# Kernel tuning notes

Measured on AMD Instinct MI355X. Metric: run time of the kernel, lower is better.

Reference implementation:

```python
import jax, jax.numpy as jnp
import numpy as np

N_USERS = 20000
N_ITEMS = 20000
H0, H1, H2 = 256, 512, 256  # hidden = [256, 512, 256]
B = 4096
LN_EPS = 1e-5


def _ln(x, g, b):
    m = jnp.mean(x, axis=-1, keepdims=True)
    v = jnp.mean(jnp.square(x - m), axis=-1, keepdims=True)
    return (x - m) * jax.lax.rsqrt(v + LN_EPS) * g + b


def setup_inputs() -> dict:
    key = jax.random.key(0)
    ks = jax.random.split(key, 12)
    s = 0.02
    inp = {
        "user_idx": jax.random.randint(ks[0], (B,), 0, N_USERS),
        "item_idx": jax.random.randint(ks[1], (B,), 0, N_ITEMS),
        # (n_users+1, n_items+1) binary interaction matrix, stored as bool
        "interactions": jax.random.bernoulli(ks[2], 0.05, (N_USERS + 1, N_ITEMS + 1)),
        # proj_u / proj_i (bias=False), torch Linear layout (out, in)
        "Wu": jax.random.normal(ks[3], (H0, N_ITEMS), jnp.float32) * s,
        "Wi": jax.random.normal(ks[4], (H0, N_USERS), jnp.float32) * s,
        # rep_u: Linear(H0,H1)+LN+ReLU, Linear(H1,H2)+LN+ReLU (dropout=eval identity)
        "W1": jax.random.normal(ks[5], (H1, H0), jnp.float32) * s,
        "b1": jnp.zeros((H1,), jnp.float32),
        "g1": jnp.ones((H1,), jnp.float32),
        "be1": jnp.zeros((H1,), jnp.float32),
        "W2": jax.random.normal(ks[6], (H2, H1), jnp.float32) * s,
        "b2": jnp.zeros((H2,), jnp.float32),
        "g2": jnp.ones((H2,), jnp.float32),
        "be2": jnp.zeros((H2,), jnp.float32),
        # logit layer
        "Wl": jax.random.normal(ks[7], (1, H2), jnp.float32) * s,
        "bl": jnp.zeros((1,), jnp.float32),
    }
    return inp


def reference(user_idx, item_idx, interactions, Wu, Wi, W1, b1, g1, be1,
              W2, b2, g2, be2, Wl, bl):
    b_arange = jnp.arange(user_idx.shape[0])

    # --- user history embedding: gather row, zero target item, project, MLP ---
    u_slice = interactions[user_idx, :-1].astype(jnp.float32)      # (B, n_items)
    u_slice = u_slice.at[b_arange, item_idx].set(0.0)
    u = u_slice @ Wu.T                                             # (B, H0)
    u = jax.nn.relu(_ln(u @ W1.T + b1, g1, be1))                   # (B, H1)
    user_rep = jax.nn.relu(_ln(u @ W2.T + b2, g2, be2))            # (B, H2)

    # --- item history embedding: gather column, zero target user, project ---
    i_slice = interactions.T[item_idx][:, :-1].astype(jnp.float32)  # (B, n_users)
    i_slice = i_slice.at[b_arange, user_idx].set(0.0)
    item_rep = i_slice @ Wi.T                                      # (B, H0); rep_i is an empty Sequential in source

    pred_vector = user_rep * item_rep                              # (B, H2) == (B, H0)
    logit = (pred_vector @ Wl.T + bl).squeeze(-1)                  # (B,)
    return logit
```

## Files before the change

### kernel.cpp

```cpp
#include <hip/hip_runtime.h>

#define N_USERS 20000
#define N_ITEMS 20000
#define NI1     20001
#define HB      4096
#define H0      256
#define H1      512
#define H2      256
#define PKW     632
#define PKB     (PKW*4)
#define NWF     12501251
#define PADN    20224

typedef unsigned short u16;
typedef unsigned char  u8;
typedef unsigned int   u32;
typedef unsigned long long u64;

typedef __attribute__((ext_vector_type(8))) __bf16 bf16x8;
typedef __attribute__((ext_vector_type(4))) float  f32x4;

__device__ __forceinline__ u16 f2bf(float f) {
  u32 u = __float_as_uint(f);
  u32 r = (u + 0x7FFFu + ((u >> 16) & 1u)) >> 16;
  return (u16)r;
}

__device__ __forceinline__ void gload16(const u16* gp, u16* lp) {
  __builtin_amdgcn_global_load_lds(
      (const __attribute__((address_space(1))) u32*)gp,
      (__attribute__((address_space(3))) u32*)lp, 16, 0, 0);
}

__global__ __launch_bounds__(256) void k_detect(const u8* __restrict__ inter,
                                                int* __restrict__ flag) {
  __shared__ u32 cnt[4];
  if (threadIdx.x < 4) cnt[threadIdx.x] = 0;
  __syncthreads();
  u32 loc0 = 0, loc1 = 0, loc2 = 0, loc3 = 0;
  for (int i = threadIdx.x; i < 16384; i += 256) {
    u32 w = ((const u32*)inter)[i];
    loc0 += (w & 0x000000FFu) ? 1u : 0u;
    loc1 += (w & 0x0000FF00u) ? 1u : 0u;
    loc2 += (w & 0x00FF0000u) ? 1u : 0u;
    loc3 += (w & 0xFF000000u) ? 1u : 0u;
  }
  atomicAdd(&cnt[0], loc0); atomicAdd(&cnt[1], loc1);
  atomicAdd(&cnt[2], loc2); atomicAdd(&cnt[3], loc3);
  __syncthreads();
  if (threadIdx.x == 0) {
    int lay;
    if (cnt[1] != 0)      lay = 0;
    else if (cnt[0] != 0) lay = 1;
    else                  lay = 2;
    *flag = lay;
  }
}

__global__ __launch_bounds__(256) void k_packF(const u8* __restrict__ inter,
                                               u32* __restrict__ pkF,
                                               const int* __restrict__ flag) {
  int lay = *flag;
  __shared__ u32 nibs[4][8][64];
  const size_t TE = (size_t)NI1 * NI1;
  const int NG = (int)((TE + 8191) / 8192);
  int wave = threadIdx.x >> 6, lane = threadIdx.x & 63;
  const u32* base32 = (const u32*)inter;
  for (int g = blockIdx.x; g < NG; g += gridDim.x) {
    size_t E0 = (size_t)g * 8192 + (size_t)wave * 2048;
    bool full = ((size_t)(g + 1) * 8192) <= TE;
    if (lay != 0) {
      if (full) {
        #pragma unroll
        for (int t = 0; t < 8; ++t) {
          size_t e = E0 + (size_t)t * 256 + lane * 4;
          uint4 v = *(const uint4*)(base32 + e);
          nibs[wave][t][lane] = (v.x ? 1u : 0u) | (v.y ? 2u : 0u) |
                                (v.z ? 4u : 0u) | (v.w ? 8u : 0u);
        }
      } else {
        #pragma unroll
        for (int t = 0; t < 8; ++t) {
          size_t e = E0 + (size_t)t * 256 + lane * 4;
          u32 n = 0;
          #pragma unroll
          for (int c = 0; c < 4; ++c)
            if (e + c < TE && base32[e + c]) n |= 1u << c;
          nibs[wave][t][lane] = n;
        }
      }
    } else {
      #pragma unroll
      for (int t = 0; t < 8; ++t) {
        size_t e = E0 + (size_t)t * 256 + lane * 4;
        u32 n = 0;
        #pragma unroll
        for (int c = 0; c < 4; ++c)
          if (e + c < TE && inter[e + c]) n |= 1u << c;
        nibs[wave][t][lane] = n;
      }
    }
    __syncthreads();
    {
      int t = lane >> 3, j = lane & 7;
      u32 wrd = 0;
      #pragma unroll
      for (int k = 0; k < 8; ++k) wrd |= nibs[wave][t][8 * j + k] << (4 * k);
      size_t wg = (size_t)g * 256 + wave * 64 + lane;
      if (wg < NWF) pkF[wg] = wrd;
    }
    __syncthreads();
  }
}

__global__ __launch_bounds__(256) void k_realign(const u32* __restrict__ pkF,
                                                 u32* __restrict__ pk) {
  int r = blockIdx.x;
  int base = 625 * r + (r >> 5);
  int s = r & 31;
  for (int w = threadIdx.x; w < PKW; w += 256) {
    u32 val = 0;
    if (w < 625) {
      u32 lo = pkF[base + w];
      u32 hi = pkF[base + w + 1];
      val = s ? ((lo >> s) | (hi << (32 - s))) : lo;
    }
    pk[(size_t)r * PKW + w] = val;
  }
}

#define HDSTEP(J, M)                                      \
  _Pragma("unroll")                                       \
  for (int k = 0; k < 32; ++k) if (!(k & J)) {            \
    u32 tt = (a[k] ^ (a[k | J] >> J)) & M;                \
    a[k] ^= tt; a[k | J] ^= tt << J;                      \
  }

__global__ __launch_bounds__(256) void k_bitT(const u32* __restrict__ pk,
                                              u32* __restrict__ pkT) {
  __shared__ u32 buf[512 * 17];
  int t = threadIdx.x;
  int vt = blockIdx.x % 40, wt = blockIdx.x / 40;
  int v0 = vt * 16, wc0 = wt * 16;
  int lw = t & 15, lr = t >> 4;
  for (int ch = 0; ch < 32; ++ch) {
    int rloc = ch * 16 + lr;
    int R = v0 * 32 + rloc;
    int W = wc0 + lw;
    u32 val = 0;
    if (R < N_USERS && W < PKW) val = pk[(size_t)R * PKW + W];
    buf[rloc * 17 + lw] = val;
  }
  __syncthreads();
  u32 a[32];
  #pragma unroll
  for (int j = 0; j < 32; ++j) a[j] = buf[(lr * 32 + j) * 17 + lw];
  HDSTEP(16, 0x0000FFFFu)
  HDSTEP(8,  0x00FF00FFu)
  HDSTEP(4,  0x0F0F0F0Fu)
  HDSTEP(2,  0x33333333u)
  HDSTEP(1,  0x55555555u)
  __syncthreads();
  #pragma unroll
  for (int i = 0; i < 32; ++i) buf[(i * 16 + lw) * 17 + lr] = __brev(a[31 - i]);
  __syncthreads();
  for (int ch = 0; ch < 32; ++ch) {
    int rloc = ch * 16 + lr;
    int C = wc0 * 32 + rloc;
    int V = v0 + lw;
    if (C < N_ITEMS && V < PKW)
      pkT[(size_t)C * PKW + V] = buf[((rloc & 31) * 16 + (rloc >> 5)) * 17 + lw];
  }
}

__global__ __launch_bounds__(256) void k_convert2p(const float* __restrict__ Wu,
                                                   const float* __restrict__ Wi,
                                                   u16* __restrict__ Wub,
                                                   u16* __restrict__ Wib) {
  int r = blockIdx.x;
  const float* src = (r < 256) ? Wu : Wi;
  u16* dst = (r < 256) ? Wub : Wib;
  int rr = r & 255;
  src += (size_t)rr * N_ITEMS;
  dst += (size_t)rr * PADN;
  for (int k8 = threadIdx.x * 8; k8 < PADN; k8 += 256 * 8) {
    u64 p = 0;
    if (k8 < N_ITEMS) {
      float4 v0 = *(const float4*)(src + k8);
      float4 v1 = *(const float4*)(src + k8 + 4);
      p = (u64)f2bf(v0.x) | ((u64)f2bf(v0.y) << 16) |
          ((u64)f2bf(v0.z) << 32) | ((u64)f2bf(v0.w) << 48);
      u64 q = (u64)f2bf(v1.x) | ((u64)f2bf(v1.y) << 16) |
              ((u64)f2bf(v1.z) << 32) | ((u64)f2bf(v1.w) << 48);
      ((u64*)(dst + k8))[0] = p;
      ((u64*)(dst + k8))[1] = q;
    } else {
      ((u64*)(dst + k8))[0] = 0;
      ((u64*)(dst + k8))[1] = 0;
    }
  }
}

__global__ __launch_bounds__(256) void k_transpose2(const float* __restrict__ W1,
                                                    float* __restrict__ W1T,
                                                    const float* __restrict__ W2,
                                                    float* __restrict__ W2T) {
  __shared__ float tile[32][33];
  int bid = blockIdx.x;
  const float* in; float* out; int R, C, b;
  if (bid < 128) { in = W1; out = W1T; R = H1; C = H0; b = bid; }
  else           { in = W2; out = W2T; R = H2; C = H1; b = bid - 128; }
  int nbx = C >> 5;
  int bx = b % nbx, by = b / nbx;
  int c0 = bx * 32, r0 = by * 32;
  int lx = threadIdx.x & 31, ly = threadIdx.x >> 5;
  #pragma unroll
  for (int j = 0; j < 4; ++j)
    tile[ly + 8*j][lx] = in[(size_t)(r0 + ly + 8*j) * C + c0 + lx];
  __syncthreads();
  #pragma unroll
  for (int j = 0; j < 4; ++j)
    out[(size_t)(c0 + ly + 8*j) * R + r0 + lx] = tile[lx][ly + 8*j];
}

__global__ __launch_bounds__(1024) void k_sort(const int* __restrict__ item_idx,
                                               int* __restrict__ perm) {
  __shared__ u32 cnt[N_ITEMS];
  __shared__ u32 tsum[1024];
  int t = threadIdx.x;
  for (int i = t; i < N_ITEMS; i += 1024) cnt[i] = 0;
  __syncthreads();
  for (int b = t; b < HB; b += 1024) atomicAdd(&cnt[item_idx[b]], 1u);
  __syncthreads();
  u32 s = 0;
  int base = t * 20;
  for (int j = 0; j < 20; ++j) { int i = base + j; if (i < N_ITEMS) s += cnt[i]; }
  tsum[t] = s;
  __syncthreads();
  for (int off = 1; off < 1024; off <<= 1) {
    u32 v = (t >= off) ? tsum[t - off] : 0u;
    __syncthreads();
    tsum[t] += v;
    __syncthreads();
  }
  u32 run = tsum[t] - s;
  for (int j = 0; j < 20; ++j) {
    int i = base + j;
    if (i < N_ITEMS) { u32 c = cnt[i]; cnt[i] = run; run += c; }
  }
  __syncthreads();
  for (int b = t; b < HB; b += 1024) {
    int v = item_idx[b];
    u32 pos = atomicAdd(&cnt[v], 1u);
    perm[pos] = b;
  }
}

__global__ __launch_bounds__(256, 4) void k_gemm(
    const u32* __restrict__ pk, const u32* __restrict__ pkT,
    const int* __restrict__ user_idx, const int* __restrict__ item_idx,
    const int* __restrict__ perm,
    const u16* __restrict__ Wub, const u16* __restrict__ Wib,
    float* __restrict__ u0, float* __restrict__ u0b,
    float* __restrict__ ir, float* __restrict__ irb) {
  __shared__ __attribute__((aligned(16))) u16 Bls[2][32 * 256];
  __shared__ __attribute__((aligned(16))) uint2 lut8[16];
  __shared__ u32 pbase[128];
  __shared__ int prow[128];

  int bid = blockIdx.x;
  int kh = bid >> 9;
  int mode_item = (bid >> 8) & 1;
  int lid = bid & 255;
  int M0 = (lid >> 3) * 128;
  int N0 = (lid & 7) * 32;
  int tid = threadIdx.x;
  const u16* Wb = mode_item ? Wib : Wub;
  const u8* Pk = (const u8*)(mode_item ? pkT : pk);
  float* Cout = mode_item ? (kh ? irb : ir) : (kh ? u0b : u0);

  if (tid < 16) {
    u32 v = tid;
    lut8[tid].x = ((v & 1u) ? 0x3F80u : 0u) | ((v & 2u) ? 0x3F800000u : 0u);
    lut8[tid].y = ((v & 4u) ? 0x3F80u : 0u) | ((v & 8u) ? 0x3F800000u : 0u);
  }
  if (tid < 128) {
    int s = M0 + tid;
    if (mode_item) { int p = perm[s]; prow[tid] = p; pbase[tid] = (u32)item_idx[p] * PKB; }
    else           { prow[tid] = s;   pbase[tid] = (u32)user_idx[s] * PKB; }
  }
  __syncthreads();

  f32x4 acc[2][2];
  #pragma unroll
  for (int a = 0; a < 2; ++a)
    #pragma unroll
    for (int b = 0; b < 2; ++b)
      #pragma unroll
      for (int j = 0; j < 4; ++j) acc[a][b][j] = 0.f;

  int lane = tid & 63, wave = tid >> 6;
  int WM = wave * 32;
  int lrow = lane & 15;
  int lk8 = lane >> 4;
  int sh = lk8 * 8;

  u32 pb0 = pbase[WM + lrow];
  u32 pb1 = pbase[WM + 16 + lrow];

  const u16* gsrc[4];
  int ldso[4];
  #pragma unroll
  for (int i = 0; i < 4; ++i) {
    int id = tid + 256 * i;
    int n = id >> 5, c8 = id & 31;
    gsrc[i] = Wb + (size_t)(N0 + n) * PADN + (c8 ^ (n & 7)) * 8;
    ldso[i] = (wave * 64 + 256 * i) * 8;
  }

  int k0_beg = kh ? 10240 : 0;
  int k0_end = kh ? 20224 : 10240;

  #pragma unroll
  for (int i = 0; i < 4; ++i) gload16(gsrc[i] + k0_beg, &Bls[0][ldso[i]]);
  int bc0 = k0_beg >> 3;
  uint4 ca0l = *(const uint4*)(Pk + pb0 + bc0);
  uint4 ca0h = *(const uint4*)(Pk + pb0 + bc0 + 16);
  uint4 ca1l = *(const uint4*)(Pk + pb1 + bc0);
  uint4 ca1h = *(const uint4*)(Pk + pb1 + bc0 + 16);
  __syncthreads();

  int cur = 0;
  for (int k0 = k0_beg; k0 < k0_end; k0 += 256) {
    int k1 = k0 + 256;
    bool more = k1 < k0_end;
    uint4 na0l, na0h, na1l, na1h;
    if (more) {
      #pragma unroll
      for (int i = 0; i < 4; ++i) gload16(gsrc[i] + k1, &Bls[cur ^ 1][ldso[i]]);
      int nbc = k1 >> 3;
      na0l = *(const uint4*)(Pk + pb0 + nbc);
      na0h = *(const uint4*)(Pk + pb0 + nbc + 16);
      na1l = *(const uint4*)(Pk + pb1 + nbc);
      na1h = *(const uint4*)(Pk + pb1 + nbc + 16);
    }
    u32 qw0[8] = {ca0l.x, ca0l.y, ca0l.z, ca0l.w, ca0h.x, ca0h.y, ca0h.z, ca0h.w};
    u32 qw1[8] = {ca1l.x, ca1l.y, ca1l.z, ca1l.w, ca1h.x, ca1h.y, ca1h.z, ca1h.w};
    #pragma unroll
    for (int kki = 0; kki < 8; ++kki) {
      u32 b0 = (qw0[kki] >> sh) & 0xFFu;
      u32 b1 = (qw1[kki] >> sh) & 0xFFu;
      union { u32 w[4]; bf16x8 v; } a0, a1;
      uint2 l0 = lut8[b0 & 15u], h0 = lut8[b0 >> 4];
      uint2 l1 = lut8[b1 & 15u], h1 = lut8[b1 >> 4];
      a0.w[0] = l0.x; a0.w[1] = l0.y; a0.w[2] = h0.x; a0.w[3] = h0.y;
      a1.w[0] = l1.x; a1.w[1] = l1.y; a1.w[2] = h1.x; a1.w[3] = h1.y;
      bf16x8 bfr[2];
      #pragma unroll
      for (int fn = 0; fn < 2; ++fn) {
        int n = fn * 16 + lrow;
        bfr[fn] = *(const bf16x8*)&Bls[cur][n * 256 + ((kki * 32 + sh) ^ ((n & 7) << 3))];
      }
      acc[0][0] = __builtin_amdgcn_mfma_f32_16x16x32_bf16(a0.v, bfr[0], acc[0][0], 0, 0, 0);
      acc[0][1] = __builtin_amdgcn_mfma_f32_16x16x32_bf16(a0.v, bfr[1], acc[0][1], 0, 0, 0);
      acc[1][0] = __builtin_amdgcn_mfma_f32_16x16x32_bf16(a1.v, bfr[0], acc[1][0], 0, 0, 0);
      acc[1][1] = __builtin_amdgcn_mfma_f32_16x16x32_bf16(a1.v, bfr[1], acc[1][1], 0, 0, 0);
    }
    if (more) { ca0l = na0l; ca0h = na0h; ca1l = na1l; ca1h = na1h; }
    __syncthreads();
    cur ^= 1;
  }

  int crow0 = (lane >> 4) * 4;
  int ccol = lane & 15;
  #pragma unroll
  for (int fm = 0; fm < 2; ++fm)
    #pragma unroll
    for (int fn = 0; fn < 2; ++fn) {
      f32x4 v = acc[fm][fn];
      int col = N0 + fn * 16 + ccol;
      #pragma unroll
      for (int j = 0; j < 4; ++j) {
        int rl = WM + fm * 16 + crow0 + j;
        Cout[(size_t)prow[rl] * H0 + col] = v[j];
      }
    }
}

__global__ __launch_bounds__(256) void k_mlp(
    const u32* __restrict__ pk,
    const int* __restrict__ user_idx, const int* __restrict__ item_idx,
    const float* __restrict__ Wu, const float* __restrict__ Wi,
    const float* __restrict__ u0, const float* __restrict__ u0b,
    const float* __restrict__ ir, const float* __restrict__ irb,
    const float* __restrict__ W1T, const float* __restrict__ b1,
    const float* __restrict__ g1, const float* __restrict__ be1,
    const float* __restrict__ W2T, const float* __restrict__ b2,
    const float* __restrict__ g2, const float* __restrict__ be2,
    const float* __restrict__ Wl, const float* __restrict__ bl,
    float* __restrict__ out) {
  __shared__ __attribute__((aligned(16))) float xl[16][H0];
  __shared__ __attribute__((aligned(16))) float h1l[16][H1];
  __shared__ int flagL[16], uL[16], iL[16];

  int tid = threadIdx.x, lane = tid & 63, wave = tid >> 6;
  int b0 = blockIdx.x * 16;

  if (tid < 16) {
    int b = b0 + tid;
    int uu = user_idx[b], ii = item_idx[b];
    uL[tid] = uu; iL[tid] = ii;
    u8 byte = ((const u8*)pk)[(size_t)uu * PKB + (ii >> 3)];
    flagL[tid] = (byte >> (ii & 7)) & 1;
  }
  __syncthreads();

  for (int idx = tid; idx < 16 * H0; idx += 256) {
    int rr = idx >> 8, h = idx & 255;
    size_t o = (size_t)(b0 + rr) * H0 + h;
    float x = u0[o] + u0b[o];
    if (flagL[rr]) x -= Wu[(size_t)h * N_ITEMS + iL[rr]];
    xl[rr][h] = x;
  }
  __syncthreads();

  float a0[16], a1[16];
  #pragma unroll
  for (int rr = 0; rr < 16; ++rr) { a0[rr] = 0.f; a1[rr] = 0.f; }
  for (int k4 = 0; k4 < H0 / 4; ++k4) {
    int k = k4 * 4;
    float w0a = W1T[(size_t)(k+0)*H1 + tid], w0b = W1T[(size_t)(k+0)*H1 + tid + 256];
    float w1a = W1T[(size_t)(k+1)*H1 + tid], w1b = W1T[(size_t)(k+1)*H1 + tid + 256];
    float w2a = W1T[(size_t)(k+2)*H1 + tid], w2b = W1T[(size_t)(k+2)*H1 + tid + 256];
    float w3a = W1T[(size_t)(k+3)*H1 + tid], w3b = W1T[(size_t)(k+3)*H1 + tid + 256];
    #pragma unroll
    for (int rr = 0; rr < 16; ++rr) {
      float4 x = *(const float4*)&xl[rr][k];
      a0[rr] += x.x * w0a + x.y * w1a + x.z * w2a + x.w * w3a;
      a1[rr] += x.x * w0b + x.y * w1b + x.z * w2b + x.w * w3b;
    }
  }
  #pragma unroll
  for (int rr = 0; rr < 16; ++rr) {
    h1l[rr][tid]       = a0[rr] + b1[tid];
    h1l[rr][tid + 256] = a1[rr] + b1[tid + 256];
  }
  __syncthreads();

  for (int rr = wave; rr < 16; rr += 4) {
    float s = 0.f;
    #pragma unroll
    for (int j = 0; j < 8; ++j) s += h1l[rr][lane + 64 * j];
    #pragma unroll
    for (int off = 32; off; off >>= 1) s += __shfl_xor(s, off);
    float m = s * (1.f / H1);
    float v = 0.f;
    #pragma unroll
    for (int j = 0; j < 8; ++j) { float d = h1l[rr][lane + 64*j] - m; v += d * d; }
    #pragma unroll
    for (int off = 32; off; off >>= 1) v += __shfl_xor(v, off);
    float inv = rsqrtf(v * (1.f / H1) + 1e-5f);
    #pragma unroll
    for (int j = 0; j < 8; ++j) {
      int o = lane + 64 * j;
      float y = (h1l[rr][o] - m) * inv * g1[o] + be1[o];
      h1l[rr][o] = fmaxf(y, 0.f);
    }
  }
  __syncthreads();

  float a2[16];
  #pragma unroll
  for (int rr = 0; rr < 16; ++rr) a2[rr] = 0.f;
  for (int k4 = 0; k4 < H1 / 4; ++k4) {
    int k = k4 * 4;
    float w0 = W2T[(size_t)(k+0)*H2 + tid];
    float w1 = W2T[(size_t)(k+1)*H2 + tid];
    float w2 = W2T[(size_t)(k+2)*H2 + tid];
    float w3 = W2T[(size_t)(k+3)*H2 + tid];
    #pragma unroll
    for (int rr = 0; rr < 16; ++rr) {
      float4 x = *(const float4*)&h1l[rr][k];
      a2[rr] += x.x * w0 + x.y * w1 + x.z * w2 + x.w * w3;
    }
  }
  __syncthreads();
  #pragma unroll
  for (int rr = 0; rr < 16; ++rr) xl[rr][tid] = a2[rr] + b2[tid];
  __syncthreads();

  for (int rr = wave; rr < 16; rr += 4) {
    float s = 0.f;
    #pragma unroll
    for (int j = 0; j < 4; ++j) s += xl[rr][lane + 64 * j];
    #pragma unroll
    for (int off = 32; off; off >>= 1) s += __shfl_xor(s, off);
    float m = s * (1.f / H2);
    float v = 0.f;
    #pragma unroll
    for (int j = 0; j < 4; ++j) { float d = xl[rr][lane + 64*j] - m; v += d * d; }
    #pragma unroll
    for (int off = 32; off; off >>= 1) v += __shfl_xor(v, off);
    float inv = rsqrtf(v * (1.f / H2) + 1e-5f);
    #pragma unroll
    for (int j = 0; j < 4; ++j) {
      int o = lane + 64 * j;
      float y = (xl[rr][o] - m) * inv * g2[o] + be2[o];
      xl[rr][o] = fmaxf(y, 0.f);
    }
  }
  __syncthreads();

  for (int rr = wave; rr < 16; rr += 4) {
    int b = b0 + rr;
    int flg = flagL[rr], uu = uL[rr];
    float s = 0.f;
    #pragma unroll
    for (int j = 0; j < 4; ++j) {
      int h = lane + 64 * j;
      size_t o = (size_t)b * H0 + h;
      float irv = ir[o] + irb[o];
      if (flg) irv -= Wi[(size_t)h * N_USERS + uu];
      s += xl[rr][h] * irv * Wl[h];
    }
    #pragma unroll
    for (int off = 32; off; off >>= 1) s += __shfl_xor(s, off);
    if (lane == 0) out[b] = s + bl[0];
  }
}

extern "C" void kernel_launch(void* const* d_in, const int* in_sizes, int n_in,
                              void* d_out, int out_size, void* d_ws, size_t ws_size,
                              hipStream_t stream) {
  const int*   user_idx = (const int*)d_in[0];
  const int*   item_idx = (const int*)d_in[1];
  const u8*    inter    = (const u8*)d_in[2];
  const float* Wu  = (const float*)d_in[3];
  const float* Wi  = (const float*)d_in[4];
  const float* W1  = (const float*)d_in[5];
  const float* b1  = (const float*)d_in[6];
  const float* g1  = (const float*)d_in[7];
  const float* be1 = (const float*)d_in[8];
  const float* W2  = (const float*)d_in[9];
  const float* b2  = (const float*)d_in[10];
  const float* g2  = (const float*)d_in[11];
  const float* be2 = (const float*)d_in[12];
  const float* Wl  = (const float*)d_in[13];
  const float* bl  = (const float*)d_in[14];
  float* out = (float*)d_out;

  char* ws = (char*)d_ws;
  size_t off = 0;
  auto alloc = [&](size_t bytes) {
    size_t o = off;
    off = (off + bytes + 255) & ~(size_t)255;
    return o;
  };
  int*   flag = (int*)  (ws + alloc(4));
  u32*   pkF  = (u32*)  (ws + alloc((size_t)(NWF + 64) * 4));
  u32*   pk   = (u32*)  (ws + alloc((size_t)N_USERS * PKB));
  u32*   pkT  = (u32*)  (ws + alloc((size_t)N_ITEMS * PKB));
  u16*   Wub  = (u16*)  (ws + alloc((size_t)H0 * PADN * 2));
  u16*   Wib  = (u16*)  (ws + alloc((size_t)H0 * PADN * 2));
  float* W1T  = (float*)(ws + alloc((size_t)H0 * H1 * 4));
  float* W2T  = (float*)(ws + alloc((size_t)H1 * H2 * 4));
  float* u0   = (float*)(ws + alloc((size_t)HB * H0 * 4));
  float* u0b  = (float*)(ws + alloc((size_t)HB * H0 * 4));
  float* ir   = (float*)(ws + alloc((size_t)HB * H0 * 4));
  float* irb  = (float*)(ws + alloc((size_t)HB * H0 * 4));
  int*   perm = (int*)  (ws + alloc((size_t)HB * 4));

  k_detect<<<1, 256, 0, stream>>>(inter, flag);
  k_packF<<<3072, 256, 0, stream>>>(inter, pkF, flag);
  k_realign<<<N_USERS, 256, 0, stream>>>(pkF, pk);
  k_bitT<<<1600, 256, 0, stream>>>(pk, pkT);
  k_convert2p<<<512, 256, 0, stream>>>(Wu, Wi, Wub, Wib);
  k_transpose2<<<256, 256, 0, stream>>>(W1, W1T, W2, W2T);
  k_sort<<<1, 1024, 0, stream>>>(item_idx, perm);
  k_gemm<<<1024, 256, 0, stream>>>(pk, pkT, user_idx, item_idx, perm, Wub, Wib,
                                   u0, u0b, ir, irb);
  k_mlp<<<256, 256, 0, stream>>>(pk, user_idx, item_idx, Wu, Wi, u0, u0b, ir, irb,
                                 W1T, b1, g1, be1, W2T, b2, g2, be2, Wl, bl, out);
}
```

Baseline: 630.0 us.

## Split GEMM K dimension four ways with smaller tiles and nontemporal pack loads

The bit-packed GEMM now splits the K reduction into four partitions instead of two and launches 2048 blocks. The per-iteration K step drops from 256 to 128, which halves LDS use and lets the occupancy hint rise from 4 to 6 blocks per CU. The MLP kernel sums four partial outputs instead of two, and the pack kernel reads the large bool matrix with nontemporal loads to avoid cache pollution. In exchange there is more partial-sum traffic and more loop iterations with more barriers per unit of work.

```diff
diff --git a/kernel.cpp b/kernel.cpp
--- a/kernel.cpp
+++ b/kernel.cpp
@@ -19,6 +19,7 @@
 
 typedef __attribute__((ext_vector_type(8))) __bf16 bf16x8;
 typedef __attribute__((ext_vector_type(4))) float  f32x4;
+typedef __attribute__((ext_vector_type(4))) u32    u32x4;
 
 __device__ __forceinline__ u16 f2bf(float f) {
   u32 u = __float_as_uint(f);
@@ -74,7 +75,7 @@
         #pragma unroll
         for (int t = 0; t < 8; ++t) {
           size_t e = E0 + (size_t)t * 256 + lane * 4;
-          uint4 v = *(const uint4*)(base32 + e);
+          u32x4 v = __builtin_nontemporal_load((const u32x4*)(base32 + e));
           nibs[wave][t][lane] = (v.x ? 1u : 0u) | (v.y ? 2u : 0u) |
                                 (v.z ? 4u : 0u) | (v.w ? 8u : 0u);
         }
@@ -184,12 +185,11 @@
   src += (size_t)rr * N_ITEMS;
   dst += (size_t)rr * PADN;
   for (int k8 = threadIdx.x * 8; k8 < PADN; k8 += 256 * 8) {
-    u64 p = 0;
     if (k8 < N_ITEMS) {
       float4 v0 = *(const float4*)(src + k8);
       float4 v1 = *(const float4*)(src + k8 + 4);
-      p = (u64)f2bf(v0.x) | ((u64)f2bf(v0.y) << 16) |
-          ((u64)f2bf(v0.z) << 32) | ((u64)f2bf(v0.w) << 48);
+      u64 p = (u64)f2bf(v0.x) | ((u64)f2bf(v0.y) << 16) |
+              ((u64)f2bf(v0.z) << 32) | ((u64)f2bf(v0.w) << 48);
       u64 q = (u64)f2bf(v1.x) | ((u64)f2bf(v1.y) << 16) |
               ((u64)f2bf(v1.z) << 32) | ((u64)f2bf(v1.w) << 48);
       ((u64*)(dst + k8))[0] = p;
@@ -256,14 +256,16 @@
   }
 }
 
-__global__ __launch_bounds__(256, 4) void k_gemm(
+__global__ __launch_bounds__(256, 6) void k_gemm(
     const u32* __restrict__ pk, const u32* __restrict__ pkT,
     const int* __restrict__ user_idx, const int* __restrict__ item_idx,
     const int* __restrict__ perm,
     const u16* __restrict__ Wub, const u16* __restrict__ Wib,
-    float* __restrict__ u0, float* __restrict__ u0b,
-    float* __restrict__ ir, float* __restrict__ irb) {
-  __shared__ __attribute__((aligned(16))) u16 Bls[2][32 * 256];
+    float* __restrict__ u0a, float* __restrict__ u0b,
+    float* __restrict__ u0c, float* __restrict__ u0d,
+    float* __restrict__ ira, float* __restrict__ irb,
+    float* __restrict__ irc, float* __restrict__ ird) {
+  __shared__ __attribute__((aligned(16))) u16 Bls[2][32 * 128];
   __shared__ __attribute__((aligned(16))) uint2 lut8[16];
   __shared__ u32 pbase[128];
   __shared__ int prow[128];
@@ -277,7 +279,9 @@
   int tid = threadIdx.x;
   const u16* Wb = mode_item ? Wib : Wub;
   const u8* Pk = (const u8*)(mode_item ? pkT : pk);
-  float* Cout = mode_item ? (kh ? irb : ir) : (kh ? u0b : u0);
+  float* Cout;
+  if (mode_item) Cout = (kh == 0) ? ira : (kh == 1) ? irb : (kh == 2) ? irc : ird;
+  else           Cout = (kh == 0) ? u0a : (kh == 1) ? u0b : (kh == 2) ? u0c : u0d;
 
   if (tid < 16) {
     u32 v = tid;
@@ -308,46 +312,40 @@
   u32 pb0 = pbase[WM + lrow];
   u32 pb1 = pbase[WM + 16 + lrow];
 
-  const u16* gsrc[4];
-  int ldso[4];
-  #pragma unroll
-  for (int i = 0; i < 4; ++i) {
+  const u16* gsrc[2];
+  int ldso[2];
+  #pragma unroll
+  for (int i = 0; i < 2; ++i) {
     int id = tid + 256 * i;
-    int n = id >> 5, c8 = id & 31;
+    int n = id >> 4, c8 = id & 15;
     gsrc[i] = Wb + (size_t)(N0 + n) * PADN + (c8 ^ (n & 7)) * 8;
     ldso[i] = (wave * 64 + 256 * i) * 8;
   }
 
-  int k0_beg = kh ? 10240 : 0;
-  int k0_end = kh ? 20224 : 10240;
-
-  #pragma unroll
-  for (int i = 0; i < 4; ++i) gload16(gsrc[i] + k0_beg, &Bls[0][ldso[i]]);
-  int bc0 = k0_beg >> 3;
-  uint4 ca0l = *(const uint4*)(Pk + pb0 + bc0);
-  uint4 ca0h = *(const uint4*)(Pk + pb0 + bc0 + 16);
-  uint4 ca1l = *(const uint4*)(Pk + pb1 + bc0);
-  uint4 ca1h = *(const uint4*)(Pk + pb1 + bc0 + 16);
+  int k0_beg = kh * 5120;
+  int k0_end = (kh == 3) ? 20224 : (k0_beg + 5120);
+
+  #pragma unroll
+  for (int i = 0; i < 2; ++i) gload16(gsrc[i] + k0_beg, &Bls[0][ldso[i]]);
+  uint4 ca0 = *(const uint4*)(Pk + pb0 + (k0_beg >> 3));
+  uint4 ca1 = *(const uint4*)(Pk + pb1 + (k0_beg >> 3));
   __syncthreads();
 
   int cur = 0;
-  for (int k0 = k0_beg; k0 < k0_end; k0 += 256) {
-    int k1 = k0 + 256;
+  for (int k0 = k0_beg; k0 < k0_end; k0 += 128) {
+    int k1 = k0 + 128;
     bool more = k1 < k0_end;
-    uint4 na0l, na0h, na1l, na1h;
+    uint4 na0, na1;
     if (more) {
       #pragma unroll
-      for (int i = 0; i < 4; ++i) gload16(gsrc[i] + k1, &Bls[cur ^ 1][ldso[i]]);
-      int nbc = k1 >> 3;
-      na0l = *(const uint4*)(Pk + pb0 + nbc);
-      na0h = *(const uint4*)(Pk + pb0 + nbc + 16);
-      na1l = *(const uint4*)(Pk + pb1 + nbc);
-      na1h = *(const uint4*)(Pk + pb1 + nbc + 16);
-    }
-    u32 qw0[8] = {ca0l.x, ca0l.y, ca0l.z, ca0l.w, ca0h.x, ca0h.y, ca0h.z, ca0h.w};
-    u32 qw1[8] = {ca1l.x, ca1l.y, ca1l.z, ca1l.w, ca1h.x, ca1h.y, ca1h.z, ca1h.w};
-    #pragma unroll
-    for (int kki = 0; kki < 8; ++kki) {
+      for (int i = 0; i < 2; ++i) gload16(gsrc[i] + k1, &Bls[cur ^ 1][ldso[i]]);
+      na0 = *(const uint4*)(Pk + pb0 + (k1 >> 3));
+      na1 = *(const uint4*)(Pk + pb1 + (k1 >> 3));
+    }
+    u32 qw0[4] = {ca0.x, ca0.y, ca0.z, ca0.w};
+    u32 qw1[4] = {ca1.x, ca1.y, ca1.z, ca1.w};
+    #pragma unroll
+    for (int kki = 0; kki < 4; ++kki) {
       u32 b0 = (qw0[kki] >> sh) & 0xFFu;
       u32 b1 = (qw1[kki] >> sh) & 0xFFu;
       union { u32 w[4]; bf16x8 v; } a0, a1;
@@ -359,14 +357,14 @@
       #pragma unroll
       for (int fn = 0; fn < 2; ++fn) {
         int n = fn * 16 + lrow;
-        bfr[fn] = *(const bf16x8*)&Bls[cur][n * 256 + ((kki * 32 + sh) ^ ((n & 7) << 3))];
+        bfr[fn] = *(const bf16x8*)&Bls[cur][n * 128 + ((kki * 32 + sh) ^ ((n & 7) << 3))];
       }
       acc[0][0] = __builtin_amdgcn_mfma_f32_16x16x32_bf16(a0.v, bfr[0], acc[0][0], 0, 0, 0);
       acc[0][1] = __builtin_amdgcn_mfma_f32_16x16x32_bf16(a0.v, bfr[1], acc[0][1], 0, 0, 0);
       acc[1][0] = __builtin_amdgcn_mfma_f32_16x16x32_bf16(a1.v, bfr[0], acc[1][0], 0, 0, 0);
       acc[1][1] = __builtin_amdgcn_mfma_f32_16x16x32_bf16(a1.v, bfr[1], acc[1][1], 0, 0, 0);
     }
-    if (more) { ca0l = na0l; ca0h = na0h; ca1l = na1l; ca1h = na1h; }
+    if (more) { ca0 = na0; ca1 = na1; }
     __syncthreads();
     cur ^= 1;
   }
@@ -391,8 +389,10 @@
     const u32* __restrict__ pk,
     const int* __restrict__ user_idx, const int* __restrict__ item_idx,
     const float* __restrict__ Wu, const float* __restrict__ Wi,
-    const float* __restrict__ u0, const float* __restrict__ u0b,
-    const float* __restrict__ ir, const float* __restrict__ irb,
+    const float* __restrict__ u0a, const float* __restrict__ u0b,
+    const float* __restrict__ u0c, const float* __restrict__ u0d,
+    const float* __restrict__ ira, const float* __restrict__ irb,
+    const float* __restrict__ irc, const float* __restrict__ ird,
     const float* __restrict__ W1T, const float* __restrict__ b1,
     const float* __restrict__ g1, const float* __restrict__ be1,
     const float* __restrict__ W2T, const float* __restrict__ b2,
@@ -418,7 +418,7 @@
   for (int idx = tid; idx < 16 * H0; idx += 256) {
     int rr = idx >> 8, h = idx & 255;
     size_t o = (size_t)(b0 + rr) * H0 + h;
-    float x = u0[o] + u0b[o];
+    float x = (u0a[o] + u0b[o]) + (u0c[o] + u0d[o]);
     if (flagL[rr]) x -= Wu[(size_t)h * N_ITEMS + iL[rr]];
     xl[rr][h] = x;
   }
@@ -519,7 +519,7 @@
     for (int j = 0; j < 4; ++j) {
       int h = lane + 64 * j;
       size_t o = (size_t)b * H0 + h;
-      float irv = ir[o] + irb[o];
+      float irv = (ira[o] + irb[o]) + (irc[o] + ird[o]);
       if (flg) irv -= Wi[(size_t)h * N_USERS + uu];
       s += xl[rr][h] * irv * Wl[h];
     }
@@ -564,10 +564,14 @@
   u16*   Wib  = (u16*)  (ws + alloc((size_t)H0 * PADN * 2));
   float* W1T  = (float*)(ws + alloc((size_t)H0 * H1 * 4));
   float* W2T  = (float*)(ws + alloc((size_t)H1 * H2 * 4));
-  float* u0   = (float*)(ws + alloc((size_t)HB * H0 * 4));
+  float* u0a  = (float*)(ws + alloc((size_t)HB * H0 * 4));
   float* u0b  = (float*)(ws + alloc((size_t)HB * H0 * 4));
-  float* ir   = (float*)(ws + alloc((size_t)HB * H0 * 4));
+  float* u0c  = (float*)(ws + alloc((size_t)HB * H0 * 4));
+  float* u0d  = (float*)(ws + alloc((size_t)HB * H0 * 4));
+  float* ira  = (float*)(ws + alloc((size_t)HB * H0 * 4));
   float* irb  = (float*)(ws + alloc((size_t)HB * H0 * 4));
+  float* irc  = (float*)(ws + alloc((size_t)HB * H0 * 4));
+  float* ird  = (float*)(ws + alloc((size_t)HB * H0 * 4));
   int*   perm = (int*)  (ws + alloc((size_t)HB * 4));
 
   k_detect<<<1, 256, 0, stream>>>(inter, flag);
@@ -577,8 +581,9 @@
   k_convert2p<<<512, 256, 0, stream>>>(Wu, Wi, Wub, Wib);
   k_transpose2<<<256, 256, 0, stream>>>(W1, W1T, W2, W2T);
   k_sort<<<1, 1024, 0, stream>>>(item_idx, perm);
-  k_gemm<<<1024, 256, 0, stream>>>(pk, pkT, user_idx, item_idx, perm, Wub, Wib,
-                                   u0, u0b, ir, irb);
-  k_mlp<<<256, 256, 0, stream>>>(pk, user_idx, item_idx, Wu, Wi, u0, u0b, ir, irb,
+  k_gemm<<<2048, 256, 0, stream>>>(pk, pkT, user_idx, item_idx, perm, Wub, Wib,
+                                   u0a, u0b, u0c, u0d, ira, irb, irc, ird);
+  k_mlp<<<256, 256, 0, stream>>>(pk, user_idx, item_idx, Wu, Wi,
+                                 u0a, u0b, u0c, u0d, ira, irb, irc, ird,
                                  W1T, b1, g1, be1, W2T, b2, g2, be2, Wl, bl, out);
 }
```

Result: faster. 584.1 us, median of 2 (-7.3%).
